# Performance work log

Hardware: AMD Instinct MI355X
Metric: run time of the kernel (lower is better)

The kernel has to match this reference:

```python
import jax, jax.numpy as jnp
import numpy as np
from jax import lax

N_QUBITS = 12
N_LAYERS = 5
DIM = 2 ** N_QUBITS
EPS = 1e-5


def _linear(x, W, b):
    return x @ W.T + b


def _bn(x, g, b):
    # BatchNorm1d in training mode: biased batch statistics
    mu = jnp.mean(x, axis=0)
    var = jnp.var(x, axis=0)
    return g * (x - mu) * lax.rsqrt(var + EPS) + b


def _leaky(x):
    return jax.nn.leaky_relu(x, 0.01)


def _gate_matrices(w):
    # w: (L, Q, 3) -> composite U3 @ RZ @ RY @ RX per (layer, qubit): (L, Q, 2, 2) complex64
    a, b, c = w[..., 0], w[..., 1], w[..., 2]
    ca = jnp.cos(a / 2).astype(jnp.complex64)
    sa = jnp.sin(a / 2).astype(jnp.complex64)
    cb = jnp.cos(b / 2).astype(jnp.complex64)
    sb = jnp.sin(b / 2).astype(jnp.complex64)
    zero = jnp.zeros_like(ca)

    def mat(m00, m01, m10, m11):
        return jnp.stack([jnp.stack([m00, m01], -1), jnp.stack([m10, m11], -1)], -2)

    RX = mat(ca, -1j * sa, -1j * sa, ca)
    RY = mat(cb, -sb, sb, cb)
    ez = jnp.exp(-0.5j * c.astype(jnp.complex64))
    RZ = mat(ez, zero, zero, jnp.conj(ez))
    eip = jnp.exp(1j * b.astype(jnp.complex64))
    eid = jnp.exp(1j * c.astype(jnp.complex64))
    U3 = mat(ca, -eid * sa, eip * sa, eip * eid * ca)  # pennylane U3(theta=a, phi=b, delta=c)
    mm = lambda A, B: jnp.einsum('lqab,lqbc->lqac', A, B)
    return mm(U3, mm(RZ, mm(RY, RX)))


def _apply1q(state, U, w):
    # state: (B, 2, ..., 2); U: (2, 2) shared across batch
    s = jnp.moveaxis(state, 1 + w, -1)
    s = jnp.einsum('...a,ca->...c', s, U)
    return jnp.moveaxis(s, -1, 1 + w)


def _cnot(state, c, t):
    s = jnp.moveaxis(state, (1 + c, 1 + t), (-2, -1))
    s = jnp.stack([s[..., 0, :], s[..., 1, ::-1]], axis=-2)
    return jnp.moveaxis(s, (-2, -1), (1 + c, 1 + t))


def _quantum(x_pre, qw):
    # Batched statevector simulation of the pennylane circuit. x_pre: (B, 12)
    B = x_pre.shape[0]
    half = x_pre * (jnp.pi / 2)  # RY(x*pi) from |0> -> [cos(x*pi/2), sin(x*pi/2)]
    vec = jnp.stack([jnp.cos(half), jnp.sin(half)], axis=-1).astype(jnp.complex64)  # (B, Q, 2)
    state = vec[:, 0]
    for q in range(1, N_QUBITS):
        state = jnp.einsum('b...,bq->b...q', state, vec[:, q])  # (B, 2, ..., 2)
    G = _gate_matrices(qw)
    for l in range(N_LAYERS):
        for q in range(N_QUBITS):
            state = _apply1q(state, G[l, q], q)
        if l % 2 == 0:
            for q in range(N_QUBITS - 1):
                state = _cnot(state, q, q + 1)
            state = _cnot(state, N_QUBITS - 1, 0)
        else:
            for q in range(0, N_QUBITS, 2):
                state = _cnot(state, q, (q + N_QUBITS // 2) % N_QUBITS)
    probs = jnp.abs(state.reshape(B, DIM)) ** 2
    idx = np.arange(DIM)
    bits = (idx[None, :] >> (N_QUBITS - 1 - np.arange(N_QUBITS))[:, None]) & 1  # (Q, DIM)
    zsigns = jnp.asarray(1.0 - 2.0 * bits, dtype=jnp.float32)
    zvals = probs @ zsigns.T  # (B, Q) PauliZ expectations
    xvals = []
    for q in range(N_QUBITS // 2):  # PauliX expectations on first Q/2 wires
        s = jnp.moveaxis(state, 1 + q, -1).reshape(B, DIM // 2, 2)
        xvals.append(2.0 * jnp.sum(jnp.real(jnp.conj(s[..., 0]) * s[..., 1]), axis=1))
    return jnp.concatenate([zvals, jnp.stack(xvals, axis=1)], axis=1)  # (B, 18)


def setup_inputs():
    key = jax.random.key(0)
    ks = jax.random.split(key, 16)
    B, NF = 4096, 64

    def W(k, o, i):
        return jax.random.normal(k, (o, i), jnp.float32) * (1.0 / np.sqrt(i))

    z = lambda n: jnp.zeros((n,), jnp.float32)
    o = lambda n: jnp.ones((n,), jnp.float32)
    return {
        'x': jax.random.normal(ks[0], (B, NF), jnp.float32),
        'Ws': W(ks[1], 128, NF), 'bs': z(128),
        'W1': W(ks[2], 256, NF), 'b1': z(256), 'g1': o(256), 'be1': z(256),
        'W2': W(ks[3], 128, 256), 'b2': z(128), 'g2': o(128), 'be2': z(128),
        'W3': W(ks[4], 64, 128), 'b3': z(64), 'g3': o(64), 'be3': z(64),
        'Wp': W(ks[5], N_QUBITS, 64), 'bp': z(N_QUBITS),
        'qw': jax.random.normal(ks[6], (N_LAYERS, N_QUBITS, 3), jnp.float32) * 0.1,
        'Wq1': W(ks[7], 128, 18), 'bq1': z(128), 'gq1': o(128), 'beq1': z(128),
        'Wq2': W(ks[8], 64, 128), 'bq2': z(64), 'gq2': o(64), 'beq2': z(64),
        'Wo1': W(ks[9], 32, 64), 'bo1': z(32),
        'Wo2': W(ks[10], 1, 32), 'bo2': z(1),
    }


def reference(x, Ws, bs, W1, b1, g1, be1, W2, b2, g2, be2, W3, b3, g3, be3,
              Wp, bp, qw, Wq1, bq1, gq1, beq1, Wq2, bq2, gq2, beq2,
              Wo1, bo1, Wo2, bo2):
    skip = _linear(x, Ws, bs)
    x1 = _leaky(_bn(_linear(x, W1, b1), g1, be1))          # dropout is eval-mode identity
    x2 = _leaky(_bn(_linear(x1, W2, b2), g2, be2))
    x3 = _leaky(_bn(_linear(x2, W3, b3), g3, be3)) + 0.1 * x1[:, :64]
    x_pre = jnp.tanh(_linear(x3, Wp, bp))
    q_out = lax.stop_gradient(_quantum(x_pre, qw))         # torch detaches the quantum path
    p1 = _leaky(_bn(_linear(q_out, Wq1, bq1), gq1, beq1)) + skip
    p2 = _leaky(_bn(_linear(p1, Wq2, bq2), gq2, beq2))
    return _linear(_leaky(_linear(p2, Wo1, bo1)), Wo2, bo2)  # (B, 1)
```

## Files before the change

kernel.cpp:

```cpp
#include <hip/hip_runtime.h>
#include <math.h>

#define LEAKY(v) ((v) > 0.f ? (v) : 0.01f * (v))

typedef float f2v __attribute__((ext_vector_type(2)));

__device__ __forceinline__ void cmm2(const float* Ar, const float* Ai,
                                     const float* Br, const float* Bi,
                                     float* Cr, float* Ci) {
#pragma unroll
  for (int r = 0; r < 2; r++)
#pragma unroll
    for (int c = 0; c < 2; c++) {
      float xr = 0.f, xi = 0.f;
#pragma unroll
      for (int k = 0; k < 2; k++) {
        float ar = Ar[r*2+k], ai = Ai[r*2+k];
        float br = Br[k*2+c], bi = Bi[k*2+c];
        xr += ar*br - ai*bi;
        xi += ar*bi + ai*br;
      }
      Cr[r*2+c] = xr; Ci[r*2+c] = xi;
    }
}

__global__ __launch_bounds__(256) void prep_k(const float* __restrict__ qw,
                                              float* __restrict__ gates,
                                              float* __restrict__ stats) {
  int t = threadIdx.x;
  for (int i = t; i < 1280; i += 256) stats[i] = 0.f;
  if (t < 60) {
    float a = qw[t*3+0], b = qw[t*3+1], c = qw[t*3+2];
    float ca = cosf(0.5f*a), sa = sinf(0.5f*a);
    float cb = cosf(0.5f*b), sb = sinf(0.5f*b);
    float RXr[4] = {ca, 0.f, 0.f, ca};
    float RXi[4] = {0.f, -sa, -sa, 0.f};
    float RYr[4] = {cb, -sb, sb, cb};
    float RYi[4] = {0.f, 0.f, 0.f, 0.f};
    float hc = 0.5f*c;
    float RZr[4] = {cosf(hc), 0.f, 0.f, cosf(hc)};
    float RZi[4] = {-sinf(hc), 0.f, 0.f, sinf(hc)};
    float epr = cosf(b), epi = sinf(b);
    float edr = cosf(c), edi = sinf(c);
    float eer = epr*edr - epi*edi, eei = epr*edi + epi*edr;
    float U3r[4] = {ca, -edr*sa, epr*sa, eer*ca};
    float U3i[4] = {0.f, -edi*sa, epi*sa, eei*ca};
    float T1r[4],T1i[4],T2r[4],T2i[4],Gr[4],Gi[4];
    cmm2(RYr,RYi, RXr,RXi, T1r,T1i);
    cmm2(RZr,RZi, T1r,T1i, T2r,T2i);
    cmm2(U3r,U3i, T2r,T2i, Gr,Gi);
#pragma unroll
    for (int m = 0; m < 4; m++) {
      gates[t*8 + 2*m]     = Gr[m];
      gates[t*8 + 2*m + 1] = Gi[m];
    }
  }
}

__device__ __forceinline__ void load_chunk(
    int tid, int r0, int c0, int kc, int K, int N,
    const float* __restrict__ A1, int ld1,
    const float* __restrict__ A2, int ld2, float scale2,
    bool lk1, bool lk2, const float* __restrict__ W,
    const float* sc1, const float* sh1,
    const float* sc2, const float* sh2,
    float* pa, float* pw) {
#pragma unroll
  for (int i = 0; i < 8; i++) {
    int t = tid + 256*i;
    int lr = t >> 6, lk = t & 63;
    int k = kc + lk;
    float av = 0.f;
    if (k < K) {
      float v1 = A1[(size_t)(r0+lr)*ld1 + k];
      v1 = sc1[k]*v1 + sh1[k];
      if (lk1) v1 = LEAKY(v1);
      av = v1;
      if (A2) {
        float v2 = A2[(size_t)(r0+lr)*ld2 + k];
        v2 = sc2[k]*v2 + sh2[k];
        if (lk2) v2 = LEAKY(v2);
        av += scale2 * v2;
      }
    }
    pa[i] = av;
  }
#pragma unroll
  for (int i = 0; i < 16; i++) {
    int t = tid + 256*i;
    int lr = t >> 6, lk = t & 63;
    int k = kc + lk;
    float wv = 0.f;
    if (k < K && c0 + lr < N) wv = W[(size_t)(c0+lr)*K + k];
    pw[i] = wv;
  }
}

__global__ __launch_bounds__(256) void gemm_f(
    const float* __restrict__ A1, const float* __restrict__ st1,
    const float* __restrict__ g1, const float* __restrict__ be1, int ld1,
    const float* __restrict__ A2, const float* __restrict__ st2,
    const float* __restrict__ g2, const float* __restrict__ be2, int ld2,
    float scale2,
    const float* __restrict__ W, const float* __restrict__ bias,
    float* __restrict__ C, float* __restrict__ statsOut, int N, int K) {
  __shared__ float As[32][65];
  __shared__ float Bs[64][65];
  __shared__ float sc1[256], sh1[256];
  __shared__ float sc2[128], sh2[128];
  const int r0 = blockIdx.x * 32;
  const int c0 = blockIdx.y * 64;
  const int tid = threadIdx.x;
  const int ty = tid >> 4, tx = tid & 15;
  const bool lk1 = (st1 != nullptr);
  const bool lk2 = (st2 != nullptr);
  for (int k = tid; k < K; k += 256) {
    if (lk1) {
      float mean = st1[2*k] * (1.f/4096.f);
      float var  = st1[2*k+1] * (1.f/4096.f) - mean*mean;
      float s = g1[k] * rsqrtf(var + 1e-5f);
      sc1[k] = s; sh1[k] = be1[k] - mean*s;
    } else { sc1[k] = 1.f; sh1[k] = 0.f; }
    if (A2 && k < 128) {
      if (lk2) {
        float mean = st2[2*k] * (1.f/4096.f);
        float var  = st2[2*k+1] * (1.f/4096.f) - mean*mean;
        float s = g2[k] * rsqrtf(var + 1e-5f);
        sc2[k] = s; sh2[k] = be2[k] - mean*s;
      } else { sc2[k] = 1.f; sh2[k] = 0.f; }
    }
  }
  __syncthreads();
  float acc[2][4] = {};
  float pa[8], pw[16];
  load_chunk(tid, r0, c0, 0, K, N, A1, ld1, A2, ld2, scale2,
             lk1, lk2, W, sc1, sh1, sc2, sh2, pa, pw);
  for (int kc = 0; kc < K; kc += 64) {
#pragma unroll
    for (int i = 0; i < 8; i++)  { int t = tid + 256*i; As[t>>6][t&63] = pa[i]; }
#pragma unroll
    for (int i = 0; i < 16; i++) { int t = tid + 256*i; Bs[t>>6][t&63] = pw[i]; }
    __syncthreads();
    if (kc + 64 < K)
      load_chunk(tid, r0, c0, kc + 64, K, N, A1, ld1, A2, ld2, scale2,
                 lk1, lk2, W, sc1, sh1, sc2, sh2, pa, pw);
#pragma unroll 16
    for (int kk = 0; kk < 64; kk++) {
      float ar[2], wr[4];
      ar[0] = As[ty*2][kk];
      ar[1] = As[ty*2+1][kk];
#pragma unroll
      for (int j = 0; j < 4; j++) wr[j] = Bs[tx*4+j][kk];
#pragma unroll
      for (int i = 0; i < 2; i++)
#pragma unroll
        for (int j = 0; j < 4; j++)
          acc[i][j] = fmaf(ar[i], wr[j], acc[i][j]);
    }
    __syncthreads();
  }
  float bv[4];
#pragma unroll
  for (int j = 0; j < 4; j++) {
    int c = c0 + tx*4 + j;
    bv[j] = (c < N) ? bias[c] : 0.f;
  }
#pragma unroll
  for (int i = 0; i < 2; i++) {
    int r = r0 + ty*2 + i;
#pragma unroll
    for (int j = 0; j < 4; j++) {
      int c = c0 + tx*4 + j;
      if (c < N) C[(size_t)r*N + c] = acc[i][j] + bv[j];
    }
  }
  if (statsOut) {
#pragma unroll
    for (int j = 0; j < 4; j++) {
      float s = 0.f, q = 0.f;
#pragma unroll
      for (int i = 0; i < 2; i++) {
        float v = acc[i][j] + bv[j];
        s += v; q += v*v;
      }
      As[ty][tx*4+j] = s;
      Bs[ty][tx*4+j] = q;
    }
    __syncthreads();
    if (tid < 64) {
      float s = 0.f, q = 0.f;
#pragma unroll
      for (int t = 0; t < 16; t++) { s += As[t][tid]; q += Bs[t][tid]; }
      int c = c0 + tid;
      if (c < N) {
        atomicAdd(&statsOut[2*c], s);
        atomicAdd(&statsOut[2*c+1], q);
      }
    }
  }
}

__device__ __forceinline__ int SWZi(int i) { return i ^ ((i >> 4) & 15); }
__device__ __forceinline__ int LINV_E(int i) {
  return i ^ ((i >> 1) & 0x7FF) ^ ((i & 1) ? 0xC00 : 0);
}
__device__ __forceinline__ int LINV_O(int i) {
  int hi = i & 0xAAA;
  return (i & 0x555) | ((hi ^ (hi << 6)) & 0xA80) | ((hi >> 6) & 0x2A);
}

template<int B>
__device__ __forceinline__ void gate16(f2v* a, const float* __restrict__ g) {
  const float g00r=g[0], g00i=g[1], g01r=g[2], g01i=g[3];
  const float g10r=g[4], g10i=g[5], g11r=g[6], g11i=g[7];
#pragma unroll
  for (int m = 0; m < 8; m++) {
    const int l0 = ((m >> B) << (B+1)) | (m & ((1<<B)-1));
    const int l1 = l0 | (1 << B);
    f2v A = a[l0], Bv = a[l1];
    f2v Ai; Ai.x = -A.y;  Ai.y = A.x;
    f2v Bi; Bi.x = -Bv.y; Bi.y = Bv.x;
    a[l0] = g00r*A + (g00i*Ai + (g01r*Bv + g01i*Bi));
    a[l1] = g10r*A + (g10i*Ai + (g11r*Bv + g11i*Bi));
  }
}

__global__ __launch_bounds__(256, 4) void quantum_k(const float* __restrict__ zpre,
                                                    const float* __restrict__ gates,
                                                    float* __restrict__ qout) {
  __shared__ f2v st[4096];
  float* stf = (float*)st;
  const int tid = threadIdx.x, b = blockIdx.x;
  if (tid < 12) {
    float xp = tanhf(zpre[b*12 + tid]);
    float h = xp * 1.57079632679489662f;
    stf[tid] = cosf(h);
    stf[12 + tid] = sinf(h);
  }
  __syncthreads();
  float cs[12], sn[12];
#pragma unroll
  for (int q = 0; q < 12; q++) { cs[q] = stf[q]; sn[q] = stf[12+q]; }
  __syncthreads();
  f2v a[16];
  {
    float pre = 1.f;
#pragma unroll
    for (int q = 0; q < 8; q++) pre *= ((tid >> (7-q)) & 1) ? sn[q] : cs[q];
#pragma unroll
    for (int l = 0; l < 16; l++) {
      float v = pre;
      v *= (l & 8) ? sn[8]  : cs[8];
      v *= (l & 4) ? sn[9]  : cs[9];
      v *= (l & 2) ? sn[10] : cs[10];
      v *= (l & 1) ? sn[11] : cs[11];
      a[l].x = v; a[l].y = 0.f;
    }
  }
  const int mA    = tid & 15;
  const int baseA = (tid << 4) | mA;
  const int baseB = ((tid >> 4) << 8) | mA;
  const int baseC = tid ^ ((tid >> 4) & 15);
  const int gE    = SWZi(LINV_E(tid << 4));
  const int gO    = SWZi(LINV_O(tid << 4));
  for (int layer = 0; layer < 5; layer++) {
    const float* gl = gates + layer * 96;
    gate16<3>(a, gl + 64); gate16<2>(a, gl + 72);
    gate16<1>(a, gl + 80); gate16<0>(a, gl + 88);
#pragma unroll
    for (int l = 0; l < 16; l++) st[baseA ^ l] = a[l];
    __syncthreads();
#pragma unroll
    for (int l = 0; l < 16; l++) a[l] = st[baseB ^ ((l << 4) | l)];
    gate16<3>(a, gl + 32); gate16<2>(a, gl + 40);
    gate16<1>(a, gl + 48); gate16<0>(a, gl + 56);
#pragma unroll
    for (int l = 0; l < 16; l++) st[baseB ^ ((l << 4) | l)] = a[l];
    __syncthreads();
#pragma unroll
    for (int l = 0; l < 16; l++) a[l] = st[baseC ^ (l << 8)];
    gate16<3>(a, gl +  0); gate16<2>(a, gl +  8);
    gate16<1>(a, gl + 16); gate16<0>(a, gl + 24);
#pragma unroll
    for (int l = 0; l < 16; l++) st[baseC ^ (l << 8)] = a[l];
    __syncthreads();
    if ((layer & 1) == 0) {
#pragma unroll
      for (int l = 0; l < 16; l++) a[l] = st[gE ^ SWZi(LINV_E(l))];
    } else {
#pragma unroll
      for (int l = 0; l < 16; l++) a[l] = st[gO ^ SWZi(LINV_O(l))];
    }
    __syncthreads();
  }
#pragma unroll
  for (int l = 0; l < 16; l++) st[baseA ^ l] = a[l];
  __syncthreads();
  float pl[16], tot = 0.f;
#pragma unroll
  for (int l = 0; l < 16; l++) { pl[l] = a[l].x*a[l].x + a[l].y*a[l].y; tot += pl[l]; }
  float part[18];
#pragma unroll
  for (int q = 0; q < 8; q++) part[q] = ((tid >> (7-q)) & 1) ? -tot : tot;
#pragma unroll
  for (int q = 8; q < 12; q++) {
    const int bit = 11 - q;
    float s = 0.f;
#pragma unroll
    for (int l = 0; l < 16; l++) s += ((l >> bit) & 1) ? -pl[l] : pl[l];
    part[q] = s;
  }
#pragma unroll
  for (int q = 0; q < 6; q++) {
    const int bt = 7 - q;
    float s = 0.f;
    if (((tid >> bt) & 1) == 0) {
      const int tid2 = tid | (1 << bt);
      const int baseA2 = (tid2 << 4) | (tid2 & 15);
#pragma unroll
      for (int l = 0; l < 16; l++) {
        f2v bb = st[baseA2 ^ l];
        s += a[l].x*bb.x + a[l].y*bb.y;
      }
    }
    part[12+q] = 2.f * s;
  }
  __syncthreads();
#pragma unroll
  for (int j = 0; j < 18; j++) {
    float v = part[j];
#pragma unroll
    for (int m = 1; m < 64; m <<= 1) v += __shfl_xor(v, m);
    if ((tid & 63) == 0) stf[(tid >> 6)*18 + j] = v;
  }
  __syncthreads();
  if (tid < 18) qout[b*18 + tid] = stf[tid] + stf[18+tid] + stf[36+tid] + stf[54+tid];
}

__global__ __launch_bounds__(256) void final_k(const float* __restrict__ P2,
                                               const float* __restrict__ stats,
                                               const float* __restrict__ g,
                                               const float* __restrict__ be,
                                               const float* __restrict__ Wo1,
                                               const float* __restrict__ bo1,
                                               const float* __restrict__ Wo2,
                                               const float* __restrict__ bo2,
                                               float* __restrict__ out) {
  __shared__ float sc[64], sh[64];
  int tid = threadIdx.x;
  if (tid < 64) {
    float mean = stats[2*tid] * (1.f/4096.f);
    float var  = stats[2*tid+1] * (1.f/4096.f) - mean*mean;
    float s = g[tid] * rsqrtf(var + 1e-5f);
    sc[tid] = s; sh[tid] = be[tid] - mean*s;
  }
  __syncthreads();
  int row = blockIdx.x*8 + (tid >> 5);
  int o = tid & 31;
  float acc = 0.f;
#pragma unroll 8
  for (int k = 0; k < 64; k++) {
    float v = sc[k]*P2[(size_t)row*64 + k] + sh[k];
    v = LEAKY(v);
    acc = fmaf(v, Wo1[o*64 + k], acc);
  }
  float h = acc + bo1[o];
  h = LEAKY(h);
  float v = h * Wo2[o];
#pragma unroll
  for (int m = 1; m < 32; m <<= 1) v += __shfl_xor(v, m);
  if (o == 0) out[row] = v + bo2[0];
}

extern "C" void kernel_launch(void* const* d_in, const int* in_sizes, int n_in,
                              void* d_out, int out_size, void* d_ws, size_t ws_size,
                              hipStream_t stream) {
  (void)in_sizes; (void)n_in; (void)out_size; (void)ws_size;
  const float* x   = (const float*)d_in[0];
  const float* Wsk = (const float*)d_in[1];
  const float* bs  = (const float*)d_in[2];
  const float* W1  = (const float*)d_in[3];
  const float* b1  = (const float*)d_in[4];
  const float* g1  = (const float*)d_in[5];
  const float* be1 = (const float*)d_in[6];
  const float* W2  = (const float*)d_in[7];
  const float* b2  = (const float*)d_in[8];
  const float* g2  = (const float*)d_in[9];
  const float* be2 = (const float*)d_in[10];
  const float* W3  = (const float*)d_in[11];
  const float* b3  = (const float*)d_in[12];
  const float* g3  = (const float*)d_in[13];
  const float* be3 = (const float*)d_in[14];
  const float* Wp  = (const float*)d_in[15];
  const float* bp  = (const float*)d_in[16];
  const float* qw  = (const float*)d_in[17];
  const float* Wq1 = (const float*)d_in[18];
  const float* bq1 = (const float*)d_in[19];
  const float* gq1 = (const float*)d_in[20];
  const float* beq1= (const float*)d_in[21];
  const float* Wq2 = (const float*)d_in[22];
  const float* bq2 = (const float*)d_in[23];
  const float* gq2 = (const float*)d_in[24];
  const float* beq2= (const float*)d_in[25];
  const float* Wo1 = (const float*)d_in[26];
  const float* bo1 = (const float*)d_in[27];
  const float* Wo2 = (const float*)d_in[28];
  const float* bo2 = (const float*)d_in[29];
  float* out = (float*)d_out;
  float* ws = (float*)d_ws;

  float* GATES = ws;
  float* ST1 = ws + 480;
  float* ST2 = ST1 + 512;
  float* ST3 = ST2 + 256;
  float* SQ1 = ST3 + 128;
  float* SQ2 = SQ1 + 256;
  float* SKIP = ws + 2048;
  float* BUF1 = SKIP + 4096*128;
  float* BUF2 = BUF1 + 4096*256;
  float* BUF3 = BUF2 + 4096*128;
  float* ZP   = BUF3 + 4096*64;
  float* QOUT = ZP + 4096*12;

  dim3 blk(256);
  prep_k<<<1, blk, 0, stream>>>(qw, GATES, ST1);
  gemm_f<<<dim3(128,2), blk, 0, stream>>>(x, nullptr,nullptr,nullptr, 64,
      nullptr,nullptr,nullptr,nullptr, 0, 0.f, Wsk, bs, SKIP, nullptr, 128, 64);
  gemm_f<<<dim3(128,4), blk, 0, stream>>>(x, nullptr,nullptr,nullptr, 64,
      nullptr,nullptr,nullptr,nullptr, 0, 0.f, W1, b1, BUF1, ST1, 256, 64);
  gemm_f<<<dim3(128,2), blk, 0, stream>>>(BUF1, ST1, g1, be1, 256,
      nullptr,nullptr,nullptr,nullptr, 0, 0.f, W2, b2, BUF2, ST2, 128, 256);
  gemm_f<<<dim3(128,1), blk, 0, stream>>>(BUF2, ST2, g2, be2, 128,
      nullptr,nullptr,nullptr,nullptr, 0, 0.f, W3, b3, BUF3, ST3, 64, 128);
  gemm_f<<<dim3(128,1), blk, 0, stream>>>(BUF3, ST3, g3, be3, 64,
      BUF1, ST1, g1, be1, 256, 0.1f, Wp, bp, ZP, nullptr, 12, 64);
  quantum_k<<<dim3(4096), blk, 0, stream>>>(ZP, GATES, QOUT);
  gemm_f<<<dim3(128,2), blk, 0, stream>>>(QOUT, nullptr,nullptr,nullptr, 18,
      nullptr,nullptr,nullptr,nullptr, 0, 0.f, Wq1, bq1, BUF2, SQ1, 128, 18);
  gemm_f<<<dim3(128,1), blk, 0, stream>>>(BUF2, SQ1, gq1, beq1, 128,
      SKIP, nullptr, nullptr, nullptr, 128, 1.0f, Wq2, bq2, BUF3, SQ2, 64, 128);
  final_k<<<dim3(512), blk, 0, stream>>>(BUF3, SQ2, gq2, beq2, Wo1, bo1, Wo2, bo2, out);
}
```

Baseline: 446.6 us.

## Merge skip and first-layer GEMMs; fold projection into quantum kernel

The skip GEMM and the first hidden GEMM, which both read x, now run as one launch with a 6-row-block grid, where blocks dispatch on blockIdx.y. The projection GEMM (BN3, leaky, residual mix, 64x12 linear, tanh) moves into the per-sample prologue of the quantum kernel, so its separate launch and the ZP buffer round trip go away. This removes two kernel launches and one global intermediate. In exchange, each quantum block redoes the BN scale/shift computation and a small serial dot product in its prologue. The stats buffers are now treated as one contiguous region, which prep_k is assumed to zero.

```diff
diff --git a/kernel.cpp b/kernel.cpp
--- a/kernel.cpp
+++ b/kernel.cpp
@@ -57,6 +57,13 @@
   }
 }
 
+struct GemmLds {
+  float As[32][65];
+  float Bs[64][65];
+  float sc1[256], sh1[256];
+  float sc2[128], sh2[128];
+};
+
 __device__ __forceinline__ void load_chunk(
     int tid, int r0, int c0, int kc, int K, int N,
     const float* __restrict__ A1, int ld1,
@@ -96,7 +103,8 @@
   }
 }
 
-__global__ __launch_bounds__(256) void gemm_f(
+__device__ __forceinline__ void gemm_body(
+    GemmLds& L, int bx, int by,
     const float* __restrict__ A1, const float* __restrict__ st1,
     const float* __restrict__ g1, const float* __restrict__ be1, int ld1,
     const float* __restrict__ A2, const float* __restrict__ st2,
@@ -104,12 +112,8 @@
     float scale2,
     const float* __restrict__ W, const float* __restrict__ bias,
     float* __restrict__ C, float* __restrict__ statsOut, int N, int K) {
-  __shared__ float As[32][65];
-  __shared__ float Bs[64][65];
-  __shared__ float sc1[256], sh1[256];
-  __shared__ float sc2[128], sh2[128];
-  const int r0 = blockIdx.x * 32;
-  const int c0 = blockIdx.y * 64;
+  const int r0 = bx * 32;
+  const int c0 = by * 64;
   const int tid = threadIdx.x;
   const int ty = tid >> 4, tx = tid & 15;
   const bool lk1 = (st1 != nullptr);
@@ -119,38 +123,38 @@
       float mean = st1[2*k] * (1.f/4096.f);
       float var  = st1[2*k+1] * (1.f/4096.f) - mean*mean;
       float s = g1[k] * rsqrtf(var + 1e-5f);
-      sc1[k] = s; sh1[k] = be1[k] - mean*s;
-    } else { sc1[k] = 1.f; sh1[k] = 0.f; }
+      L.sc1[k] = s; L.sh1[k] = be1[k] - mean*s;
+    } else { L.sc1[k] = 1.f; L.sh1[k] = 0.f; }
     if (A2 && k < 128) {
       if (lk2) {
         float mean = st2[2*k] * (1.f/4096.f);
         float var  = st2[2*k+1] * (1.f/4096.f) - mean*mean;
         float s = g2[k] * rsqrtf(var + 1e-5f);
-        sc2[k] = s; sh2[k] = be2[k] - mean*s;
-      } else { sc2[k] = 1.f; sh2[k] = 0.f; }
+        L.sc2[k] = s; L.sh2[k] = be2[k] - mean*s;
+      } else { L.sc2[k] = 1.f; L.sh2[k] = 0.f; }
     }
   }
   __syncthreads();
   float acc[2][4] = {};
   float pa[8], pw[16];
   load_chunk(tid, r0, c0, 0, K, N, A1, ld1, A2, ld2, scale2,
-             lk1, lk2, W, sc1, sh1, sc2, sh2, pa, pw);
+             lk1, lk2, W, L.sc1, L.sh1, L.sc2, L.sh2, pa, pw);
   for (int kc = 0; kc < K; kc += 64) {
 #pragma unroll
-    for (int i = 0; i < 8; i++)  { int t = tid + 256*i; As[t>>6][t&63] = pa[i]; }
-#pragma unroll
-    for (int i = 0; i < 16; i++) { int t = tid + 256*i; Bs[t>>6][t&63] = pw[i]; }
+    for (int i = 0; i < 8; i++)  { int t = tid + 256*i; L.As[t>>6][t&63] = pa[i]; }
+#pragma unroll
+    for (int i = 0; i < 16; i++) { int t = tid + 256*i; L.Bs[t>>6][t&63] = pw[i]; }
     __syncthreads();
     if (kc + 64 < K)
       load_chunk(tid, r0, c0, kc + 64, K, N, A1, ld1, A2, ld2, scale2,
-                 lk1, lk2, W, sc1, sh1, sc2, sh2, pa, pw);
+                 lk1, lk2, W, L.sc1, L.sh1, L.sc2, L.sh2, pa, pw);
 #pragma unroll 16
     for (int kk = 0; kk < 64; kk++) {
       float ar[2], wr[4];
-      ar[0] = As[ty*2][kk];
-      ar[1] = As[ty*2+1][kk];
-#pragma unroll
-      for (int j = 0; j < 4; j++) wr[j] = Bs[tx*4+j][kk];
+      ar[0] = L.As[ty*2][kk];
+      ar[1] = L.As[ty*2+1][kk];
+#pragma unroll
+      for (int j = 0; j < 4; j++) wr[j] = L.Bs[tx*4+j][kk];
 #pragma unroll
       for (int i = 0; i < 2; i++)
 #pragma unroll
@@ -183,14 +187,14 @@
         float v = acc[i][j] + bv[j];
         s += v; q += v*v;
       }
-      As[ty][tx*4+j] = s;
-      Bs[ty][tx*4+j] = q;
+      L.As[ty][tx*4+j] = s;
+      L.Bs[ty][tx*4+j] = q;
     }
     __syncthreads();
     if (tid < 64) {
       float s = 0.f, q = 0.f;
 #pragma unroll
-      for (int t = 0; t < 16; t++) { s += As[t][tid]; q += Bs[t][tid]; }
+      for (int t = 0; t < 16; t++) { s += L.As[t][tid]; q += L.Bs[t][tid]; }
       int c = c0 + tid;
       if (c < N) {
         atomicAdd(&statsOut[2*c], s);
@@ -198,6 +202,36 @@
       }
     }
   }
+}
+
+__global__ __launch_bounds__(256) void gemm_f(
+    const float* __restrict__ A1, const float* __restrict__ st1,
+    const float* __restrict__ g1, const float* __restrict__ be1, int ld1,
+    const float* __restrict__ A2, const float* __restrict__ st2,
+    const float* __restrict__ g2, const float* __restrict__ be2, int ld2,
+    float scale2,
+    const float* __restrict__ W, const float* __restrict__ bias,
+    float* __restrict__ C, float* __restrict__ statsOut, int N, int K) {
+  __shared__ GemmLds L;
+  gemm_body(L, blockIdx.x, blockIdx.y, A1, st1, g1, be1, ld1,
+            A2, st2, g2, be2, ld2, scale2, W, bias, C, statsOut, N, K);
+}
+
+__global__ __launch_bounds__(256) void z1skip_k(
+    const float* __restrict__ x,
+    const float* __restrict__ W1, const float* __restrict__ b1,
+    float* __restrict__ BUF1, float* __restrict__ ST1,
+    const float* __restrict__ Wsk, const float* __restrict__ bs,
+    float* __restrict__ SKIP) {
+  __shared__ GemmLds L;
+  if (blockIdx.y < 4)
+    gemm_body(L, blockIdx.x, blockIdx.y, x, nullptr,nullptr,nullptr, 64,
+              nullptr,nullptr,nullptr,nullptr, 0, 0.f,
+              W1, b1, BUF1, ST1, 256, 64);
+  else
+    gemm_body(L, blockIdx.x, blockIdx.y - 4, x, nullptr,nullptr,nullptr, 64,
+              nullptr,nullptr,nullptr,nullptr, 0, 0.f,
+              Wsk, bs, SKIP, nullptr, 128, 64);
 }
 
 __device__ __forceinline__ int SWZi(int i) { return i ^ ((i >> 4) & 15); }
@@ -225,22 +259,54 @@
   }
 }
 
-__global__ __launch_bounds__(256, 4) void quantum_k(const float* __restrict__ zpre,
-                                                    const float* __restrict__ gates,
-                                                    float* __restrict__ qout) {
+__global__ __launch_bounds__(256, 4) void quantum_k(
+    const float* __restrict__ z3buf,
+    const float* __restrict__ z1buf,
+    const float* __restrict__ stats,
+    const float* __restrict__ g1, const float* __restrict__ be1,
+    const float* __restrict__ g3, const float* __restrict__ be3,
+    const float* __restrict__ Wp, const float* __restrict__ bp,
+    const float* __restrict__ gates,
+    float* __restrict__ qout) {
   __shared__ f2v st[4096];
   float* stf = (float*)st;
   const int tid = threadIdx.x, b = blockIdx.x;
+  if (tid < 64) {
+    const float* ST3 = stats + 768;
+    float mean = ST3[2*tid] * (1.f/4096.f);
+    float var  = ST3[2*tid+1] * (1.f/4096.f) - mean*mean;
+    float s = g3[tid] * rsqrtf(var + 1e-5f);
+    stf[tid] = s; stf[64+tid] = be3[tid] - mean*s;
+  } else if (tid < 128) {
+    int k = tid - 64;
+    float mean = stats[2*k] * (1.f/4096.f);
+    float var  = stats[2*k+1] * (1.f/4096.f) - mean*mean;
+    float s = g1[k] * rsqrtf(var + 1e-5f);
+    stf[128+k] = s; stf[192+k] = be1[k] - mean*s;
+  }
+  __syncthreads();
+  if (tid < 64) {
+    int k = tid;
+    float v3 = stf[k]*z3buf[(size_t)b*64 + k] + stf[64+k];
+    v3 = LEAKY(v3);
+    float v1 = stf[128+k]*z1buf[(size_t)b*256 + k] + stf[192+k];
+    v1 = LEAKY(v1);
+    stf[256+k] = v3 + 0.1f*v1;
+  }
+  __syncthreads();
   if (tid < 12) {
-    float xp = tanhf(zpre[b*12 + tid]);
+    float acc = bp[tid];
+#pragma unroll 8
+    for (int k = 0; k < 64; k++) acc = fmaf(stf[256+k], Wp[tid*64+k], acc);
+    float xp = tanhf(acc);
     float h = xp * 1.57079632679489662f;
-    stf[tid] = cosf(h);
-    stf[12 + tid] = sinf(h);
+    stf[320+tid] = cosf(h);
+    stf[332+tid] = sinf(h);
   }
   __syncthreads();
   float cs[12], sn[12];
 #pragma unroll
-  for (int q = 0; q < 12; q++) { cs[q] = stf[q]; sn[q] = stf[12+q]; }
+  for (int q = 0; q < 12; q++) { cs[q] = stf[320+q]; sn[q] = stf[332+q]; }
   __syncthreads();
   f2v a[16];
   {
@@ -410,31 +476,27 @@
   float* ws = (float*)d_ws;
 
   float* GATES = ws;
-  float* ST1 = ws + 480;
-  float* ST2 = ST1 + 512;
-  float* ST3 = ST2 + 256;
-  float* SQ1 = ST3 + 128;
-  float* SQ2 = SQ1 + 256;
+  float* STATS = ws + 480;
+  float* ST1 = STATS;
+  float* ST2 = STATS + 512;
+  float* ST3 = STATS + 768;
+  float* SQ1 = STATS + 896;
+  float* SQ2 = STATS + 1152;
   float* SKIP = ws + 2048;
   float* BUF1 = SKIP + 4096*128;
   float* BUF2 = BUF1 + 4096*256;
   float* BUF3 = BUF2 + 4096*128;
-  float* ZP   = BUF3 + 4096*64;
-  float* QOUT = ZP + 4096*12;
+  float* QOUT = BUF3 + 4096*64 + 4096*12;
 
   dim3 blk(256);
-  prep_k<<<1, blk, 0, stream>>>(qw, GATES, ST1);
-  gemm_f<<<dim3(128,2), blk, 0, stream>>>(x, nullptr,nullptr,nullptr, 64,
-      nullptr,nullptr,nullptr,nullptr, 0, 0.f, Wsk, bs, SKIP, nullptr, 128, 64);
-  gemm_f<<<dim3(128,4), blk, 0, stream>>>(x, nullptr,nullptr,nullptr, 64,
-      nullptr,nullptr,nullptr,nullptr, 0, 0.f, W1, b1, BUF1, ST1, 256, 64);
+  prep_k<<<1, blk, 0, stream>>>(qw, GATES, STATS);
+  z1skip_k<<<dim3(128,6), blk, 0, stream>>>(x, W1, b1, BUF1, ST1, Wsk, bs, SKIP);
   gemm_f<<<dim3(128,2), blk, 0, stream>>>(BUF1, ST1, g1, be1, 256,
       nullptr,nullptr,nullptr,nullptr, 0, 0.f, W2, b2, BUF2, ST2, 128, 256);
   gemm_f<<<dim3(128,1), blk, 0, stream>>>(BUF2, ST2, g2, be2, 128,
       nullptr,nullptr,nullptr,nullptr, 0, 0.f, W3, b3, BUF3, ST3, 64, 128);
-  gemm_f<<<dim3(128,1), blk, 0, stream>>>(BUF3, ST3, g3, be3, 64,
-      BUF1, ST1, g1, be1, 256, 0.1f, Wp, bp, ZP, nullptr, 12, 64);
-  quantum_k<<<dim3(4096), blk, 0, stream>>>(ZP, GATES, QOUT);
+  quantum_k<<<dim3(4096), blk, 0, stream>>>(BUF3, BUF1, STATS,
+      g1, be1, g3, be3, Wp, bp, GATES, QOUT);
   gemm_f<<<dim3(128,2), blk, 0, stream>>>(QOUT, nullptr,nullptr,nullptr, 18,
       nullptr,nullptr,nullptr,nullptr, 0, 0.f, Wq1, bq1, BUF2, SQ1, 128, 18);
   gemm_f<<<dim3(128,1), blk, 0, stream>>>(BUF2, SQ1, gq1, beq1, 128,
```

Result: faster. 427.0 us (-4.4%).
